# Kernel optimization log

Measured on AMD Instinct MI355X. Metric: run time of the kernel, lower is better.

## Reference

```python
import jax, jax.numpy as jnp
import numpy as np

EPS = 1e-5
HEADS = 4
DIMK = 16
DIMU = 4
R = 23


def _bn_eval(x, g, b):
    # BatchNorm2d in eval mode with running_mean=0, running_var=1
    return x * (g / np.sqrt(1.0 + EPS))[None, :, None, None] + b[None, :, None, None]


def _conv1x1(x, w):
    # w: (O, C) from a Conv2d(C, O, 1) weight
    return jnp.einsum('bchw,oc->bohw', x, w)


def _lambda_layer(x, wq, wk, wv, qg, qb, vg, vb, pw, pb):
    B, C, H, W = x.shape
    n = H * W
    V = wv.shape[0] // DIMU  # dim_out // heads
    q = _bn_eval(_conv1x1(x, wq), qg, qb).reshape(B, HEADS, DIMK, n)
    k = jax.nn.softmax(_conv1x1(x, wk).reshape(B, DIMU, DIMK, n), axis=-1)
    v = _bn_eval(_conv1x1(x, wv), vg, vb).reshape(B, DIMU, V, n)
    # content lambda: (B, k, v)
    lam_c = jnp.einsum('bukn,buvn->bkv', k, v)
    y_c = jnp.einsum('bhkn,bkv->bhvn', q, lam_c)
    # position lambdas: Conv3d(u, k, (1, R, R)) == 2D conv over (H, W) with v folded into batch
    v5 = v.reshape(B, DIMU, V, H, W).transpose(0, 2, 1, 3, 4).reshape(B * V, DIMU, H, W)
    p = R // 2
    lp = jax.lax.conv_general_dilated(v5, pw, (1, 1), [(p, p), (p, p)],
                                      dimension_numbers=('NCHW', 'OIHW', 'NCHW'))
    lp = lp + pb[None, :, None, None]
    lam_p = lp.reshape(B, V, DIMK, H, W).transpose(0, 2, 1, 3, 4).reshape(B, DIMK, V, n)
    y_p = jnp.einsum('bhkn,bkvn->bhvn', q, lam_p)
    return (y_c + y_p).reshape(B, HEADS * V, H, W)


def _group_norm(x, g, b, groups=8):
    B, C, H, W = x.shape
    xr = x.reshape(B, groups, C // groups, H, W)
    m = xr.mean(axis=(2, 3, 4), keepdims=True)
    var = xr.var(axis=(2, 3, 4), keepdims=True)
    xn = ((xr - m) / jnp.sqrt(var + EPS)).reshape(B, C, H, W)
    return xn * g[None, :, None, None] + b[None, :, None, None]


def setup_inputs() -> dict:
    key = jax.random.key(0)
    B, C, H, W = 4, 64, 192, 192
    V = C // HEADS
    d = {'x': jax.random.normal(jax.random.fold_in(key, 0), (B, C, H, W), jnp.float32)}
    i = 1
    for l in (1, 2, 3):
        for nm, shape, kind in [
            ('wq', (HEADS * DIMK, C), 'w'), ('wk', (DIMU * DIMK, C), 'w'), ('wv', (DIMU * V, C), 'w'),
            ('qg', (HEADS * DIMK,), 'ones'), ('qb', (HEADS * DIMK,), 'zeros'),
            ('vg', (DIMU * V,), 'ones'), ('vb', (DIMU * V,), 'zeros'),
            ('pw', (DIMK, DIMU, R, R), 'w'), ('pb', (DIMK,), 'zeros')]:
            if kind == 'w':
                d['l%d_%s' % (l, nm)] = jax.random.normal(jax.random.fold_in(key, i), shape, jnp.float32) * 0.05
            elif kind == 'ones':
                d['l%d_%s' % (l, nm)] = jnp.ones(shape, jnp.float32)
            else:
                d['l%d_%s' % (l, nm)] = jnp.zeros(shape, jnp.float32)
            i += 1
    d['gn1_g'] = jnp.ones((C,), jnp.float32); d['gn1_b'] = jnp.zeros((C,), jnp.float32)
    d['gn3_g'] = jnp.ones((C,), jnp.float32); d['gn3_b'] = jnp.zeros((C,), jnp.float32)
    d['cw'] = jax.random.normal(jax.random.fold_in(key, 99), (C, C), jnp.float32) * 0.01
    d['cb'] = jnp.zeros((C,), jnp.float32)
    return d


def reference(x,
              l1_wq, l1_wk, l1_wv, l1_qg, l1_qb, l1_vg, l1_vb, l1_pw, l1_pb,
              l2_wq, l2_wk, l2_wv, l2_qg, l2_qb, l2_vg, l2_vb, l2_pw, l2_pb,
              l3_wq, l3_wk, l3_wv, l3_qg, l3_qb, l3_vg, l3_vb, l3_pw, l3_pb,
              gn1_g, gn1_b, gn3_g, gn3_b, cw, cb):
    out = _lambda_layer(x, l1_wq, l1_wk, l1_wv, l1_qg, l1_qb, l1_vg, l1_vb, l1_pw, l1_pb)
    out = _group_norm(out, gn1_g, gn1_b)
    out = _lambda_layer(out, l2_wq, l2_wk, l2_wv, l2_qg, l2_qb, l2_vg, l2_vb, l2_pw, l2_pb)
    out = _group_norm(out, gn1_g, gn1_b)  # original code reuses gn1 here (gn2 unused)
    out = _lambda_layer(out, l3_wq, l3_wk, l3_wv, l3_qg, l3_qb, l3_vg, l3_vb, l3_pw, l3_pb)
    out = _group_norm(out, gn3_g, gn3_b)
    out = _conv1x1(out, cw) + cb[None, :, None, None]
    return out * 0.2 + x
```

## Files before the change

### kernel.cpp

```cpp
#include <hip/hip_runtime.h>

typedef unsigned short USH;
typedef __attribute__((ext_vector_type(8))) short bf16x8;
typedef __attribute__((ext_vector_type(4))) float f32x4;

#define MFMA16(a,b,c) __builtin_amdgcn_mfma_f32_16x16x32_bf16((a),(b),(c),0,0,0)

#define BB 4
#define HH 192
#define NN 36864
#define NTOT 147456
#define CSTR 120

__device__ __forceinline__ float bf2f(USH h) {
    union { unsigned int u; float f; } v; v.u = ((unsigned int)h) << 16; return v.f;
}
__device__ __forceinline__ USH f2bf(float f) {
    union { float f; unsigned int u; } v; v.f = f;
    unsigned int u = v.u;
    return (USH)((u + 0x7FFFu + ((u >> 16) & 1u)) >> 16);
}

struct PrepArgs {
    const float* wq[3]; const float* wk[3]; const float* wv[3];
    const float* qg[3]; const float* qb[3]; const float* vg[3]; const float* vb[3];
    const float* pw[3]; const float* cw;
};
__global__ void prep_all_k(PrepArgs pa, USH* __restrict__ apc, USH* __restrict__ apq,
                           float* __restrict__ biasq, USH* __restrict__ apf) {
    int bid = blockIdx.x, tid = threadIdx.x;
    if (bid < 552) {
        int L = bid / 184, cb = bid - L * 184;
        int t = cb * 256 + tid;
        if (t < 736 * 64) {
            const float* pw = pa.pw[L];
            USH* ap = apc + (size_t)L * 376832;
            int lane = t & 63, cg = t >> 6;
            int dy = cg % 23; int ru = cg / 23; int u = ru & 3; int r = ru >> 2;
            int kk = lane & 15, q8 = (lane >> 4) * 8;
            for (int j = 0; j < 8; ++j) {
                int k = q8 + j, dx = k - r - 1;
                USH w = 0;
                if (dx >= 0 && dx < 23) w = f2bf(pw[((kk * 4 + u) * 23 + dy) * 23 + dx]);
                ap[t * 8 + j] = w;
            }
        }
    } else if (bid < 570) {
        int idx = bid - 552; int L = idx / 6; int qblk = idx - L * 6;
        int t = qblk * 256 + tid;
        USH* apl = apq + (size_t)L * 12288;
        float* bl = biasq + L * 192;
        if (t < 1536) {
            int lane = t & 63, chunk = t >> 6;
            int mt = chunk >> 1, kc = chunk & 1;
            int o = mt * 16 + (lane & 15);
            int c0 = kc * 32 + (lane >> 4) * 8;
            float scale; const float* wrow;
            if (o < 64)       { scale = pa.qg[L][o]       * rsqrtf(1.0f + 1e-5f); wrow = pa.wq[L] + o * 64; }
            else if (o < 128) { scale = 1.0f;                                     wrow = pa.wk[L] + (o - 64) * 64; }
            else              { scale = pa.vg[L][o - 128] * rsqrtf(1.0f + 1e-5f); wrow = pa.wv[L] + (o - 128) * 64; }
            for (int j = 0; j < 8; ++j) apl[t * 8 + j] = f2bf(wrow[c0 + j] * scale);
        }
        if (t < 192) {
            float bvv;
            if (t < 64) bvv = pa.qb[L][t]; else if (t < 128) bvv = 0.0f; else bvv = pa.vb[L][t - 128];
            bl[t] = bvv;
        }
    } else {
        int t = (bid - 570) * 256 + tid;
        if (t < 512) {
            int lane = t & 63, chunk = t >> 6;
            int mt = chunk >> 1, kc = chunk & 1;
            int o = mt * 16 + (lane & 15);
            int c0 = kc * 32 + (lane >> 4) * 8;
            for (int j = 0; j < 8; ++j) apf[t * 8 + j] = f2bf(pa.cw[o * 64 + c0 + j]);
        }
    }
}

__global__ __launch_bounds__(256) void x_qkv_k(
    const float* __restrict__ xin, const bf16x8* __restrict__ apre, const float* __restrict__ bias,
    USH* __restrict__ qT, USH* __restrict__ kbuf, USH* __restrict__ vbuf) {
    __shared__ float tf[64][65];
    const int bid = blockIdx.x; const int b = bid / 576; const int nt = bid - b * 576; const int n0 = nt * 64;
    const int tid = threadIdx.x, lane = tid & 63, wq = tid >> 6;
    const int nl = lane & 15, quad = lane >> 4;
    bf16x8 afr[24];
    #pragma unroll
    for (int i = 0; i < 24; ++i) afr[i] = apre[i * 64 + lane];
    #pragma unroll
    for (int p = 0; p < 16; ++p) {
        int idx = p * 256 + tid; int c = idx >> 6, nn = idx & 63;
        tf[nn][c] = xin[((size_t)b * 64 + c) * NN + n0 + nn];
    }
    __syncthreads();
    bf16x8 b0, b1;
    #pragma unroll
    for (int j = 0; j < 8; ++j) {
        b0[j] = (short)f2bf(tf[wq * 16 + nl][quad * 8 + j]);
        b1[j] = (short)f2bf(tf[wq * 16 + nl][32 + quad * 8 + j]);
    }
    const int n = n0 + wq * 16 + nl;
    #pragma unroll
    for (int mt = 0; mt < 12; ++mt) {
        f32x4 acc = {0.f, 0.f, 0.f, 0.f};
        acc = MFMA16(afr[mt * 2 + 0], b0, acc);
        acc = MFMA16(afr[mt * 2 + 1], b1, acc);
        int o0 = mt * 16 + quad * 4;
        float4 bs = *(const float4*)(bias + o0);
        float v0 = acc[0] + bs.x, v1 = acc[1] + bs.y, v2 = acc[2] + bs.z, v3 = acc[3] + bs.w;
        if (mt < 4) {
            ushort4 pk; pk.x = f2bf(v0); pk.y = f2bf(v1); pk.z = f2bf(v2); pk.w = f2bf(v3);
            *(ushort4*)(qT + ((size_t)b * NN + n) * 64 + o0) = pk;
        } else if (mt < 8) {
            int ko = o0 - 64;
            kbuf[((size_t)b * 64 + ko    ) * NN + n] = f2bf(v0);
            kbuf[((size_t)b * 64 + ko + 1) * NN + n] = f2bf(v1);
            kbuf[((size_t)b * 64 + ko + 2) * NN + n] = f2bf(v2);
            kbuf[((size_t)b * 64 + ko + 3) * NN + n] = f2bf(v3);
        } else {
            int u = mt - 8, vv0 = quad * 4;
            vbuf[(((size_t)b * 16 + vv0    ) * 4 + u) * NN + n] = f2bf(v0);
            vbuf[(((size_t)b * 16 + vv0 + 1) * 4 + u) * NN + n] = f2bf(v1);
            vbuf[(((size_t)b * 16 + vv0 + 2) * 4 + u) * NN + n] = f2bf(v2);
            vbuf[(((size_t)b * 16 + vv0 + 3) * 4 + u) * NN + n] = f2bf(v3);
        }
    }
}

__global__ __launch_bounds__(1024) void softstat_k(const USH* __restrict__ kbuf,
                                                   float* __restrict__ kstat) {
    __shared__ USH row_s[NN];
    __shared__ float red[64];
    const USH* p = kbuf + (size_t)blockIdx.x * NN;
    int tid = threadIdx.x, lane = tid & 63, w = tid >> 6;
    float m = -1e30f;
    for (int i = tid * 4; i < NN; i += 4096) {
        ushort4 t4 = *(const ushort4*)(p + i);
        *(ushort4*)(row_s + i) = t4;
        m = fmaxf(m, fmaxf(fmaxf(bf2f(t4.x), bf2f(t4.y)), fmaxf(bf2f(t4.z), bf2f(t4.w))));
    }
    for (int off = 32; off; off >>= 1) m = fmaxf(m, __shfl_down(m, off));
    if (lane == 0) red[w] = m;
    __syncthreads();
    if (tid == 0) { float mm = red[0]; for (int i = 1; i < 16; ++i) mm = fmaxf(mm, red[i]); red[16] = mm; }
    __syncthreads();
    float M = red[16];
    float s = 0.f;
    for (int i = tid * 4; i < NN; i += 4096) {
        ushort4 t4 = *(const ushort4*)(row_s + i);
        s += __expf(bf2f(t4.x) - M) + __expf(bf2f(t4.y) - M)
           + __expf(bf2f(t4.z) - M) + __expf(bf2f(t4.w) - M);
    }
    for (int off = 32; off; off >>= 1) s += __shfl_down(s, off);
    if (lane == 0) red[32 + w] = s;
    __syncthreads();
    if (tid == 0) {
        float ss = 0.f;
        for (int i = 0; i < 16; ++i) ss += red[32 + i];
        kstat[blockIdx.x * 2]     = M;
        kstat[blockIdx.x * 2 + 1] = 1.0f / ss;
    }
}

__global__ __launch_bounds__(64) void lamc_stage1_k(
    const USH* __restrict__ kbuf, const USH* __restrict__ vbuf,
    const float* __restrict__ kstat, float* __restrict__ part) {
    int bid = blockIdx.x;
    int cidx = bid >> 4; int rem = bid & 15; int b = rem >> 2; int u = rem & 3;
    int lane = threadIdx.x; int nl = lane & 15, quad = lane >> 4;
    int krow = b * 64 + u * 16 + nl;
    float M = kstat[krow * 2], inv = kstat[krow * 2 + 1];
    const USH* kp = kbuf + (size_t)krow * NN + cidx * 512 + quad * 8;
    const USH* vp = vbuf + (((size_t)b * 16 + nl) * 4 + u) * NN + cidx * 512 + quad * 8;
    f32x4 acc = {0.f, 0.f, 0.f, 0.f};
    #pragma unroll 4
    for (int s = 0; s < 16; ++s) {
        bf16x8 kr = *(const bf16x8*)(kp + s * 32);
        bf16x8 va = *(const bf16x8*)(vp + s * 32);
        bf16x8 ka;
        #pragma unroll
        for (int j = 0; j < 8; ++j)
            ka[j] = (short)f2bf(__expf(bf2f((USH)kr[j]) - M) * inv);
        acc = MFMA16(ka, va, acc);
    }
    float* pout = part + ((size_t)(cidx * 4 + b) * 4 + u) * 256;
    #pragma unroll
    for (int rg = 0; rg < 4; ++rg)
        pout[nl * 16 + quad * 4 + rg] = acc[rg];
}
__global__ void lamc_stage2_k(const float* __restrict__ part, const float* __restrict__ pb,
                              float* __restrict__ lamcf) {
    int b = blockIdx.x, tid = threadIdx.x;
    float acc = 0.f;
    for (int c = 0; c < 72; ++c)
        for (int u = 0; u < 4; ++u)
            acc += part[((size_t)(c * 4 + b) * 4 + u) * 256 + tid];
    lamcf[b * 256 + tid] = acc + pb[tid & 15];
}

__global__ __launch_bounds__(256, 3) void conv_pos_fused_k(
    const USH* __restrict__ vbuf, const bf16x8* __restrict__ apre,
    const USH* __restrict__ qT, const float* __restrict__ lamcf,
    USH* __restrict__ yb, float* __restrict__ gnp2) {
    __shared__ __align__(16) USH in_s[4 * 54 * CSTR];
    __shared__ float lc_s[16];
    __shared__ float gn_s[16], gn_q[16];
    const int xh = blockIdx.x, yt = blockIdx.y, img = blockIdx.z;
    const int b = img >> 4, vvch = img & 15;
    const int tid = threadIdx.x;
    if (tid < 16) lc_s[tid] = lamcf[b * 256 + vvch * 16 + tid];
    {
        const USH* vb = vbuf + (size_t)img * 4 * NN;
        const int y0 = yt * 32 - 11, x0 = xh * 96 - 12;
        for (int i4 = tid; i4 < 6480; i4 += 256) {
            int u = i4 / 1620;
            int rem = i4 - u * 1620;
            int rr = rem / 30;
            int cc = (rem - rr * 30) * 4;
            int gy = y0 + rr, gx = x0 + cc;
            ushort4 val = {0, 0, 0, 0};
            if (gy >= 0 && gy < HH && gx >= 0 && gx <= HH - 4)
                val = *(const ushort4*)(vb + u * NN + gy * HH + gx);
            *(ushort4*)(in_s + (u * 54 + rr) * CSTR + cc) = val;
        }
    }
    __syncthreads();

    const int lane = tid & 63, wv = tid >> 6;
    const int wy = wv >> 1, wx = wv & 1;
    const int nl = lane & 15, quad = lane >> 4;
    const USH* sbase = in_s + (wy * 16 + nl) * CSTR + wx * 48 + quad * 8;
    const int ybase = yt * 32 + wy * 16 + nl;
    float lcr0 = lc_s[quad * 4], lcr1 = lc_s[quad * 4 + 1],
          lcr2 = lc_s[quad * 4 + 2], lcr3 = lc_s[quad * 4 + 3];
    const USH* qbase = qT + ((size_t)b * NN + ybase * HH) * 64 + quad * 4;
    USH* ybbase = yb + ((size_t)b * 64 + quad * 16 + vvch) * NN + ybase * HH;
    float SG = 0.f, QG = 0.f;

#define CONV_EPILOGUE(ACC, RVAL)                                                            \
    {                                                                                       \
        _Pragma("unroll")                                                                   \
        for (int xi = 0; xi < 6; ++xi) {                                                    \
            int x = xh * 96 + wx * 48 + (RVAL) + 8 * xi;                                    \
            float l0 = ACC[xi][0] + lcr0, l1 = ACC[xi][1] + lcr1;                           \
            float l2 = ACC[xi][2] + lcr2, l3 = ACC[xi][3] + lcr3;                           \
            const USH* qp = qbase + (size_t)x * 64;                                         \
            float s0, s1, s2, s3;                                                           \
            {                                                                               \
                ushort4 q4 = *(const ushort4*)(qp);                                         \
                s0 = bf2f(q4.x) * l0 + bf2f(q4.y) * l1 + bf2f(q4.z) * l2 + bf2f(q4.w) * l3; \
            }                                                                               \
            {                                                                               \
                ushort4 q4 = *(const ushort4*)(qp + 16);                                    \
                s1 = bf2f(q4.x) * l0 + bf2f(q4.y) * l1 + bf2f(q4.z) * l2 + bf2f(q4.w) * l3; \
            }                                                                               \
            {                                                                               \
                ushort4 q4 = *(const ushort4*)(qp + 32);                                    \
                s2 = bf2f(q4.x) * l0 + bf2f(q4.y) * l1 + bf2f(q4.z) * l2 + bf2f(q4.w) * l3; \
            }                                                                               \
            {                                                                               \
                ushort4 q4 = *(const ushort4*)(qp + 48);                                    \
                s3 = bf2f(q4.x) * l0 + bf2f(q4.y) * l1 + bf2f(q4.z) * l2 + bf2f(q4.w) * l3; \
            }                                                                               \
            s0 += __shfl_xor(s0, 16); s0 += __shfl_xor(s0, 32);                             \
            s1 += __shfl_xor(s1, 16); s1 += __shfl_xor(s1, 32);                             \
            s2 += __shfl_xor(s2, 16); s2 += __shfl_xor(s2, 32);                             \
            s3 += __shfl_xor(s3, 16); s3 += __shfl_xor(s3, 32);                             \
            float sel = (quad == 0) ? s0 : (quad == 1) ? s1 : (quad == 2) ? s2 : s3;        \
            USH wo = f2bf(sel);                                                             \
            ybbase[x] = wo;                                                                 \
            float wf = bf2f(wo);                                                            \
            SG += wf; QG += wf * wf;                                                        \
        }                                                                                   \
    }

#define CONV_PASS3(R0)                                                                      \
    {                                                                                       \
        f32x4 acc0[6] = {}; f32x4 acc1[6] = {}; f32x4 acc2[6] = {};                         \
        for (int u = 0; u < 4; ++u) {                                                       \
            const bf16x8* ap0 = apre + ((size_t)((R0) * 4 + u) * 23) * 64 + lane;           \
            const bf16x8* ap1 = ap0 + 4 * 23 * 64;                                          \
            const bf16x8* ap2 = ap0 + 2 * 4 * 23 * 64;                                      \
            const USH* srow = sbase + u * (54 * CSTR);                                      \
            _Pragma("unroll 2")                                                             \
            for (int dy = 0; dy < 23; ++dy) {                                               \
                bf16x8 a0 = *ap0, a1 = *ap1, a2 = *ap2;                                     \
                _Pragma("unroll")                                                           \
                for (int xi = 0; xi < 6; ++xi) {                                            \
                    bf16x8 bfr = *(const bf16x8*)(srow + 8 * xi);                           \
                    acc0[xi] = MFMA16(a0, bfr, acc0[xi]);                                   \
                    acc1[xi] = MFMA16(a1, bfr, acc1[xi]);                                   \
                    acc2[xi] = MFMA16(a2, bfr, acc2[xi]);                                   \
                }                                                                           \
                ap0 += 64; ap1 += 64; ap2 += 64; srow += CSTR;                               \
            }                                                                               \
        }                                                                                   \
        CONV_EPILOGUE(acc0, (R0))                                                           \
        CONV_EPILOGUE(acc1, (R0) + 1)                                                       \
        CONV_EPILOGUE(acc2, (R0) + 2)                                                       \
    }

    CONV_PASS3(0)
    CONV_PASS3(3)
    {
        f32x4 acc0[6] = {}; f32x4 acc1[6] = {};
        for (int u = 0; u < 4; ++u) {
            const bf16x8* ap0 = apre + ((size_t)(6 * 4 + u) * 23) * 64 + lane;
            const bf16x8* ap1 = ap0 + 4 * 23 * 64;
            const USH* srow = sbase + u * (54 * CSTR);
            #pragma unroll 2
            for (int dy = 0; dy < 23; ++dy) {
                bf16x8 a0 = *ap0, a1 = *ap1;
                #pragma unroll
                for (int xi = 0; xi < 6; ++xi) {
                    bf16x8 bfr = *(const bf16x8*)(srow + 8 * xi);
                    acc0[xi] = MFMA16(a0, bfr, acc0[xi]);
                    acc1[xi] = MFMA16(a1, bfr, acc1[xi]);
                }
                ap0 += 64; ap1 += 64; srow += CSTR;
            }
        }
        CONV_EPILOGUE(acc0, 6)
        CONV_EPILOGUE(acc1, 7)
    }
#undef CONV_PASS3
#undef CONV_EPILOGUE

    SG += __shfl_xor(SG, 1); SG += __shfl_xor(SG, 2); SG += __shfl_xor(SG, 4); SG += __shfl_xor(SG, 8);
    QG += __shfl_xor(QG, 1); QG += __shfl_xor(QG, 2); QG += __shfl_xor(QG, 4); QG += __shfl_xor(QG, 8);
    if (nl == 0) { gn_s[wv * 4 + quad] = SG; gn_q[wv * 4 + quad] = QG; }
    __syncthreads();
    if (tid < 4) {
        float s = gn_s[tid] + gn_s[4 + tid] + gn_s[8 + tid] + gn_s[12 + tid];
        float q = gn_q[tid] + gn_q[4 + tid] + gn_q[8 + tid] + gn_q[12 + tid];
        int lin = img * 12 + yt * 2 + xh;
        gnp2[lin * 8 + tid * 2]     = s;
        gnp2[lin * 8 + tid * 2 + 1] = q;
    }
}

__global__ void gn_passB_k(const float* __restrict__ gnp2, float* __restrict__ stats) {
    int t = threadIdx.x;
    if (t < 32) {
        int b = t >> 3, g = t & 7;
        int quad = g >> 1, v0 = (g & 1) * 8;
        float s = 0.f, q = 0.f;
        for (int vv = 0; vv < 8; ++vv)
            for (int tile = 0; tile < 12; ++tile) {
                const float* p = gnp2 + ((size_t)((b * 16 + v0 + vv) * 12 + tile)) * 8 + quad * 2;
                s += p[0]; q += p[1];
            }
        float mean = s / 294912.0f;
        float var = q / 294912.0f - mean * mean;
        stats[t * 2] = mean;
        stats[t * 2 + 1] = rsqrtf(fmaxf(var, 0.0f) + 1e-5f);
    }
}

__global__ __launch_bounds__(256) void gn_qkv_k(
    const USH* __restrict__ yb, const float* __restrict__ stats,
    const float* __restrict__ gg, const float* __restrict__ gb,
    const bf16x8* __restrict__ apre, const float* __restrict__ bias,
    USH* __restrict__ qT, USH* __restrict__ kbuf, USH* __restrict__ vbuf) {
    __shared__ float tf[64][65];
    __shared__ float sc[64], sb[64];
    const int bid = blockIdx.x; const int b = bid / 576; const int nt = bid - b * 576; const int n0 = nt * 64;
    const int tid = threadIdx.x, lane = tid & 63, wq = tid >> 6;
    const int nl = lane & 15, quad = lane >> 4;
    bf16x8 afr[24];
    #pragma unroll
    for (int i = 0; i < 24; ++i) afr[i] = apre[i * 64 + lane];
    if (tid < 64) {
        int g = tid >> 3;
        float mean = stats[(b * 8 + g) * 2], rstd = stats[(b * 8 + g) * 2 + 1];
        float ga = gg[tid];
        sc[tid] = rstd * ga;
        sb[tid] = gb[tid] - mean * rstd * ga;
    }
    __syncthreads();
    #pragma unroll
    for (int p = 0; p < 4; ++p) {
        int c = p * 16 + (tid >> 4), nn = (tid & 15) * 4;
        ushort4 y4 = *(const ushort4*)(yb + ((size_t)b * 64 + c) * NN + n0 + nn);
        float scc = sc[c], sbc = sb[c];
        tf[nn][c]     = bf2f(y4.x) * scc + sbc;
        tf[nn + 1][c] = bf2f(y4.y) * scc + sbc;
        tf[nn + 2][c] = bf2f(y4.z) * scc + sbc;
        tf[nn + 3][c] = bf2f(y4.w) * scc + sbc;
    }
    __syncthreads();
    bf16x8 b0, b1;
    #pragma unroll
    for (int j = 0; j < 8; ++j) {
        b0[j] = (short)f2bf(tf[wq * 16 + nl][quad * 8 + j]);
        b1[j] = (short)f2bf(tf[wq * 16 + nl][32 + quad * 8 + j]);
    }
    const int n = n0 + wq * 16 + nl;
    #pragma unroll
    for (int mt = 0; mt < 12; ++mt) {
        f32x4 acc = {0.f, 0.f, 0.f, 0.f};
        acc = MFMA16(afr[mt * 2 + 0], b0, acc);
        acc = MFMA16(afr[mt * 2 + 1], b1, acc);
        int o0 = mt * 16 + quad * 4;
        float4 bs = *(const float4*)(bias + o0);
        float v0 = acc[0] + bs.x, v1 = acc[1] + bs.y, v2 = acc[2] + bs.z, v3 = acc[3] + bs.w;
        if (mt < 4) {
            ushort4 pk; pk.x = f2bf(v0); pk.y = f2bf(v1); pk.z = f2bf(v2); pk.w = f2bf(v3);
            *(ushort4*)(qT + ((size_t)b * NN + n) * 64 + o0) = pk;
        } else if (mt < 8) {
            int ko = o0 - 64;
            kbuf[((size_t)b * 64 + ko    ) * NN + n] = f2bf(v0);
            kbuf[((size_t)b * 64 + ko + 1) * NN + n] = f2bf(v1);
            kbuf[((size_t)b * 64 + ko + 2) * NN + n] = f2bf(v2);
            kbuf[((size_t)b * 64 + ko + 3) * NN + n] = f2bf(v3);
        } else {
            int u = mt - 8, vv0 = quad * 4;
            vbuf[(((size_t)b * 16 + vv0    ) * 4 + u) * NN + n] = f2bf(v0);
            vbuf[(((size_t)b * 16 + vv0 + 1) * 4 + u) * NN + n] = f2bf(v1);
            vbuf[(((size_t)b * 16 + vv0 + 2) * 4 + u) * NN + n] = f2bf(v2);
            vbuf[(((size_t)b * 16 + vv0 + 3) * 4 + u) * NN + n] = f2bf(v3);
        }
    }
}

__global__ __launch_bounds__(256) void gn_final_k(
    const USH* __restrict__ yb, const float* __restrict__ stats,
    const float* __restrict__ gg, const float* __restrict__ gb,
    const bf16x8* __restrict__ apre, const float* __restrict__ cb,
    const float* __restrict__ xin, float* __restrict__ out) {
    __shared__ float tf[64][65];
    __shared__ float sc[64], sb[64];
    const int bid = blockIdx.x; const int b = bid / 576; const int nt = bid - b * 576; const int n0 = nt * 64;
    const int tid = threadIdx.x, lane = tid & 63, wq = tid >> 6;
    const int nl = lane & 15, quad = lane >> 4;
    bf16x8 afr[8];
    #pragma unroll
    for (int i = 0; i < 8; ++i) afr[i] = apre[i * 64 + lane];
    if (tid < 64) {
        int g = tid >> 3;
        float mean = stats[(b * 8 + g) * 2], rstd = stats[(b * 8 + g) * 2 + 1];
        float ga = gg[tid];
        sc[tid] = rstd * ga;
        sb[tid] = gb[tid] - mean * rstd * ga;
    }
    __syncthreads();
    #pragma unroll
    for (int p = 0; p < 4; ++p) {
        int c = p * 16 + (tid >> 4), nn = (tid & 15) * 4;
        ushort4 y4 = *(const ushort4*)(yb + ((size_t)b * 64 + c) * NN + n0 + nn);
        float scc = sc[c], sbc = sb[c];
        tf[nn][c]     = bf2f(y4.x) * scc + sbc;
        tf[nn + 1][c] = bf2f(y4.y) * scc + sbc;
        tf[nn + 2][c] = bf2f(y4.z) * scc + sbc;
        tf[nn + 3][c] = bf2f(y4.w) * scc + sbc;
    }
    __syncthreads();
    bf16x8 b0, b1;
    #pragma unroll
    for (int j = 0; j < 8; ++j) {
        b0[j] = (short)f2bf(tf[wq * 16 + nl][quad * 8 + j]);
        b1[j] = (short)f2bf(tf[wq * 16 + nl][32 + quad * 8 + j]);
    }
    const int n = n0 + wq * 16 + nl;
    #pragma unroll
    for (int mt = 0; mt < 4; ++mt) {
        f32x4 acc = {0.f, 0.f, 0.f, 0.f};
        acc = MFMA16(afr[mt * 2 + 0], b0, acc);
        acc = MFMA16(afr[mt * 2 + 1], b1, acc);
        int o0 = mt * 16 + quad * 4;
        float4 cb4 = *(const float4*)(cb + o0);
        float cbv[4] = { cb4.x, cb4.y, cb4.z, cb4.w };
        #pragma unroll
        for (int rg = 0; rg < 4; ++rg) {
            int o = o0 + rg;
            float xv = xin[((size_t)b * 64 + o) * NN + n];
            out[((size_t)b * 64 + o) * NN + n] = (acc[rg] + cbv[rg]) * 0.2f + xv;
        }
    }
}

extern "C" void kernel_launch(void* const* d_in, const int* in_sizes, int n_in,
                              void* d_out, int out_size, void* d_ws, size_t ws_size,
                              hipStream_t stream) {
    (void)in_sizes; (void)n_in; (void)out_size; (void)ws_size;
    const float* x = (const float*)d_in[0];
    char* ws = (char*)d_ws;

    const size_t SZP = (size_t)NTOT * 64 * 2;
    USH*   P0 = (USH*)(ws);
    USH*   P1 = (USH*)(ws + SZP);
    USH*   P2 = (USH*)(ws + 2 * SZP);
    USH*   P3 = (USH*)(ws + 3 * SZP);
    char*  tail  = ws + 4 * SZP;
    USH*   apc   = (USH*)(tail);            tail += 753664 * 3;
    USH*   apq   = (USH*)(tail);            tail += 24576 * 3;
    float* biasq = (float*)(tail);          tail += 768 * 3;
    USH*   apf   = (USH*)(tail);            tail += 8192;
    float* lcp   = (float*)(tail);          tail += 1179648;
    float* lcf   = (float*)(tail);          tail += 4096;
    float* gnp2  = (float*)(tail);          tail += 24576;
    float* gns   = (float*)(tail);          tail += 256;
    float* kst   = (float*)(tail);

    PrepArgs pa;
    for (int L = 0; L < 3; ++L) {
        int base = 1 + L * 9;
        pa.wq[L] = (const float*)d_in[base + 0];
        pa.wk[L] = (const float*)d_in[base + 1];
        pa.wv[L] = (const float*)d_in[base + 2];
        pa.qg[L] = (const float*)d_in[base + 3];
        pa.qb[L] = (const float*)d_in[base + 4];
        pa.vg[L] = (const float*)d_in[base + 5];
        pa.vb[L] = (const float*)d_in[base + 6];
        pa.pw[L] = (const float*)d_in[base + 7];
    }
    pa.cw = (const float*)d_in[32];

    prep_all_k<<<572, 256, 0, stream>>>(pa, apc, apq, biasq, apf);

    x_qkv_k<<<2304, 256, 0, stream>>>(x, (const bf16x8*)apq, biasq, P1, P2, P3);

    for (int L = 0; L < 3; ++L) {
        const float* pb = (const float*)d_in[1 + L * 9 + 8];
        USH* kv = (L == 1) ? P0 : P2;

        softstat_k<<<256, 1024, 0, stream>>>(kv, kst);
        lamc_stage1_k<<<1152, 64, 0, stream>>>(kv, P3, kst, lcp);
        lamc_stage2_k<<<4, 256, 0, stream>>>(lcp, pb, lcf);
        dim3 cg(2, 6, 64);
        conv_pos_fused_k<<<cg, 256, 0, stream>>>(P3, (const bf16x8*)apc + (size_t)L * 47104,
                                                 P1, lcf, kv, gnp2);
        gn_passB_k<<<1, 256, 0, stream>>>(gnp2, gns);
        if (L < 2) {
            const float* gg = (const float*)d_in[28];
            const float* gb = (const float*)d_in[29];
            USH* knext = (L == 0) ? P0 : P2;
            gn_qkv_k<<<2304, 256, 0, stream>>>(kv, gns, gg, gb,
                                               (const bf16x8*)apq + (size_t)(L + 1) * 1536,
                                               biasq + (L + 1) * 192, P1, knext, P3);
        } else {
            const float* gg = (const float*)d_in[30];
            const float* gb = (const float*)d_in[31];
            gn_final_k<<<2304, 256, 0, stream>>>(kv, gns, gg, gb, (const bf16x8*)apf,
                                                 (const float*)d_in[33], x, (float*)d_out);
        }
    }
}
```

Measured before the change: 942.1 us.

## Fold lambda-content and group-norm reductions into consumer kernels, drop tiny launches

Removes the single-block lamc_stage2 and gn_passB kernels per layer. Their reductions now run redundantly inside every conv_pos_fused and gn_qkv/gn_final block. lamc_stage1 is split into 192 chunks instead of 72 to raise parallelism, which enlarges the partial buffer. The aim is to remove serialized tiny launches and their pipeline bubbles, at the cost of redundant global reads of the partials in every consumer block.

```diff
diff --git a/kernel.cpp b/kernel.cpp
--- a/kernel.cpp
+++ b/kernel.cpp
@@ -11,6 +11,7 @@
 #define NN 36864
 #define NTOT 147456
 #define CSTR 120
+#define NCH 192
 
 __device__ __forceinline__ float bf2f(USH h) {
     union { unsigned int u; float f; } v; v.u = ((unsigned int)h) << 16; return v.f;
@@ -171,11 +172,11 @@
     int lane = threadIdx.x; int nl = lane & 15, quad = lane >> 4;
     int krow = b * 64 + u * 16 + nl;
     float M = kstat[krow * 2], inv = kstat[krow * 2 + 1];
-    const USH* kp = kbuf + (size_t)krow * NN + cidx * 512 + quad * 8;
-    const USH* vp = vbuf + (((size_t)b * 16 + nl) * 4 + u) * NN + cidx * 512 + quad * 8;
+    const USH* kp = kbuf + (size_t)krow * NN + cidx * 192 + quad * 8;
+    const USH* vp = vbuf + (((size_t)b * 16 + nl) * 4 + u) * NN + cidx * 192 + quad * 8;
     f32x4 acc = {0.f, 0.f, 0.f, 0.f};
-    #pragma unroll 4
-    for (int s = 0; s < 16; ++s) {
+    #pragma unroll
+    for (int s = 0; s < 6; ++s) {
         bf16x8 kr = *(const bf16x8*)(kp + s * 32);
         bf16x8 va = *(const bf16x8*)(vp + s * 32);
         bf16x8 ka;
@@ -189,27 +190,27 @@
     for (int rg = 0; rg < 4; ++rg)
         pout[nl * 16 + quad * 4 + rg] = acc[rg];
 }
-__global__ void lamc_stage2_k(const float* __restrict__ part, const float* __restrict__ pb,
-                              float* __restrict__ lamcf) {
-    int b = blockIdx.x, tid = threadIdx.x;
-    float acc = 0.f;
-    for (int c = 0; c < 72; ++c)
-        for (int u = 0; u < 4; ++u)
-            acc += part[((size_t)(c * 4 + b) * 4 + u) * 256 + tid];
-    lamcf[b * 256 + tid] = acc + pb[tid & 15];
-}
 
 __global__ __launch_bounds__(256, 3) void conv_pos_fused_k(
     const USH* __restrict__ vbuf, const bf16x8* __restrict__ apre,
-    const USH* __restrict__ qT, const float* __restrict__ lamcf,
-    USH* __restrict__ yb, float* __restrict__ gnp2) {
+    const USH* __restrict__ qT, const float* __restrict__ lcp,
+    const float* __restrict__ pb, USH* __restrict__ yb, float* __restrict__ gnp2) {
     __shared__ __align__(16) USH in_s[4 * 54 * CSTR];
+    __shared__ float lc_red[16][16];
     __shared__ float lc_s[16];
     __shared__ float gn_s[16], gn_q[16];
     const int xh = blockIdx.x, yt = blockIdx.y, img = blockIdx.z;
     const int b = img >> 4, vvch = img & 15;
     const int tid = threadIdx.x;
-    if (tid < 16) lc_s[tid] = lamcf[b * 256 + vvch * 16 + tid];
+    {
+        int kk = tid & 15, slice = tid >> 4;
+        float s = 0.f;
+        for (int p = slice * 48; p < slice * 48 + 48; ++p) {
+            int cidx = p >> 2, u = p & 3;
+            s += lcp[((size_t)(cidx * 4 + b) * 4 + u) * 256 + vvch * 16 + kk];
+        }
+        lc_red[slice][kk] = s;
+    }
     {
         const USH* vb = vbuf + (size_t)img * 4 * NN;
         const int y0 = yt * 32 - 11, x0 = xh * 96 - 12;
@@ -224,6 +225,13 @@
                 val = *(const ushort4*)(vb + u * NN + gy * HH + gx);
             *(ushort4*)(in_s + (u * 54 + rr) * CSTR + cc) = val;
         }
+    }
+    __syncthreads();
+    if (tid < 16) {
+        float s = 0.f;
+        #pragma unroll
+        for (int sl = 0; sl < 16; ++sl) s += lc_red[sl][tid];
+        lc_s[tid] = s + pb[tid];
     }
     __syncthreads();
 
@@ -340,31 +348,14 @@
     }
 }
 
-__global__ void gn_passB_k(const float* __restrict__ gnp2, float* __restrict__ stats) {
-    int t = threadIdx.x;
-    if (t < 32) {
-        int b = t >> 3, g = t & 7;
-        int quad = g >> 1, v0 = (g & 1) * 8;
-        float s = 0.f, q = 0.f;
-        for (int vv = 0; vv < 8; ++vv)
-            for (int tile = 0; tile < 12; ++tile) {
-                const float* p = gnp2 + ((size_t)((b * 16 + v0 + vv) * 12 + tile)) * 8 + quad * 2;
-                s += p[0]; q += p[1];
-            }
-        float mean = s / 294912.0f;
-        float var = q / 294912.0f - mean * mean;
-        stats[t * 2] = mean;
-        stats[t * 2 + 1] = rsqrtf(fmaxf(var, 0.0f) + 1e-5f);
-    }
-}
-
 __global__ __launch_bounds__(256) void gn_qkv_k(
-    const USH* __restrict__ yb, const float* __restrict__ stats,
+    const USH* __restrict__ yb, const float* __restrict__ gnp2,
     const float* __restrict__ gg, const float* __restrict__ gb,
     const bf16x8* __restrict__ apre, const float* __restrict__ bias,
     USH* __restrict__ qT, USH* __restrict__ kbuf, USH* __restrict__ vbuf) {
     __shared__ float tf[64][65];
     __shared__ float sc[64], sb[64];
+    __shared__ float grs[64], grq[64], st_s[16];
     const int bid = blockIdx.x; const int b = bid / 576; const int nt = bid - b * 576; const int n0 = nt * 64;
     const int tid = threadIdx.x, lane = tid & 63, wq = tid >> 6;
     const int nl = lane & 15, quad = lane >> 4;
@@ -372,8 +363,30 @@
     #pragma unroll
     for (int i = 0; i < 24; ++i) afr[i] = apre[i * 64 + lane];
     if (tid < 64) {
+        int g = tid >> 3, vv = tid & 7;
+        int qg = g >> 1, v0 = (g & 1) * 8;
+        float s = 0.f, q = 0.f;
+        #pragma unroll
+        for (int tile = 0; tile < 12; ++tile) {
+            const float* p = gnp2 + ((size_t)((b * 16 + v0 + vv) * 12 + tile)) * 8 + qg * 2;
+            s += p[0]; q += p[1];
+        }
+        grs[tid] = s; grq[tid] = q;
+    }
+    __syncthreads();
+    if (tid < 8) {
+        float s = 0.f, q = 0.f;
+        #pragma unroll
+        for (int vv = 0; vv < 8; ++vv) { s += grs[tid * 8 + vv]; q += grq[tid * 8 + vv]; }
+        float mean = s / 294912.0f;
+        float var = q / 294912.0f - mean * mean;
+        st_s[tid * 2] = mean;
+        st_s[tid * 2 + 1] = rsqrtf(fmaxf(var, 0.0f) + 1e-5f);
+    }
+    __syncthreads();
+    if (tid < 64) {
         int g = tid >> 3;
-        float mean = stats[(b * 8 + g) * 2], rstd = stats[(b * 8 + g) * 2 + 1];
+        float mean = st_s[g * 2], rstd = st_s[g * 2 + 1];
         float ga = gg[tid];
         sc[tid] = rstd * ga;
         sb[tid] = gb[tid] - mean * rstd * ga;
@@ -425,12 +438,13 @@
 }
 
 __global__ __launch_bounds__(256) void gn_final_k(
-    const USH* __restrict__ yb, const float* __restrict__ stats,
+    const USH* __restrict__ yb, const float* __restrict__ gnp2,
     const float* __restrict__ gg, const float* __restrict__ gb,
     const bf16x8* __restrict__ apre, const float* __restrict__ cb,
     const float* __restrict__ xin, float* __restrict__ out) {
     __shared__ float tf[64][65];
     __shared__ float sc[64], sb[64];
+    __shared__ float grs[64], grq[64], st_s[16];
     const int bid = blockIdx.x; const int b = bid / 576; const int nt = bid - b * 576; const int n0 = nt * 64;
     const int tid = threadIdx.x, lane = tid & 63, wq = tid >> 6;
     const int nl = lane & 15, quad = lane >> 4;
@@ -438,8 +452,30 @@
     #pragma unroll
     for (int i = 0; i < 8; ++i) afr[i] = apre[i * 64 + lane];
     if (tid < 64) {
+        int g = tid >> 3, vv = tid & 7;
+        int qg = g >> 1, v0 = (g & 1) * 8;
+        float s = 0.f, q = 0.f;
+        #pragma unroll
+        for (int tile = 0; tile < 12; ++tile) {
+            const float* p = gnp2 + ((size_t)((b * 16 + v0 + vv) * 12 + tile)) * 8 + qg * 2;
+            s += p[0]; q += p[1];
+        }
+        grs[tid] = s; grq[tid] = q;
+    }
+    __syncthreads();
+    if (tid < 8) {
+        float s = 0.f, q = 0.f;
+        #pragma unroll
+        for (int vv = 0; vv < 8; ++vv) { s += grs[tid * 8 + vv]; q += grq[tid * 8 + vv]; }
+        float mean = s / 294912.0f;
+        float var = q / 294912.0f - mean * mean;
+        st_s[tid * 2] = mean;
+        st_s[tid * 2 + 1] = rsqrtf(fmaxf(var, 0.0f) + 1e-5f);
+    }
+    __syncthreads();
+    if (tid < 64) {
         int g = tid >> 3;
-        float mean = stats[(b * 8 + g) * 2], rstd = stats[(b * 8 + g) * 2 + 1];
+        float mean = st_s[g * 2], rstd = st_s[g * 2 + 1];
         float ga = gg[tid];
         sc[tid] = rstd * ga;
         sb[tid] = gb[tid] - mean * rstd * ga;
@@ -497,10 +533,8 @@
     USH*   apq   = (USH*)(tail);            tail += 24576 * 3;
     float* biasq = (float*)(tail);          tail += 768 * 3;
     USH*   apf   = (USH*)(tail);            tail += 8192;
-    float* lcp   = (float*)(tail);          tail += 1179648;
-    float* lcf   = (float*)(tail);          tail += 4096;
+    float* lcp   = (float*)(tail);          tail += 3145728;
     float* gnp2  = (float*)(tail);          tail += 24576;
-    float* gns   = (float*)(tail);          tail += 256;
     float* kst   = (float*)(tail);
 
     PrepArgs pa;
@@ -526,23 +560,21 @@
         USH* kv = (L == 1) ? P0 : P2;
 
         softstat_k<<<256, 1024, 0, stream>>>(kv, kst);
-        lamc_stage1_k<<<1152, 64, 0, stream>>>(kv, P3, kst, lcp);
-        lamc_stage2_k<<<4, 256, 0, stream>>>(lcp, pb, lcf);
+        lamc_stage1_k<<<NCH * 16, 64, 0, stream>>>(kv, P3, kst, lcp);
         dim3 cg(2, 6, 64);
         conv_pos_fused_k<<<cg, 256, 0, stream>>>(P3, (const bf16x8*)apc + (size_t)L * 47104,
-                                                 P1, lcf, kv, gnp2);
-        gn_passB_k<<<1, 256, 0, stream>>>(gnp2, gns);
+                                                 P1, lcp, pb, kv, gnp2);
         if (L < 2) {
             const float* gg = (const float*)d_in[28];
             const float* gb = (const float*)d_in[29];
             USH* knext = (L == 0) ? P0 : P2;
-            gn_qkv_k<<<2304, 256, 0, stream>>>(kv, gns, gg, gb,
+            gn_qkv_k<<<2304, 256, 0, stream>>>(kv, gnp2, gg, gb,
                                                (const bf16x8*)apq + (size_t)(L + 1) * 1536,
                                                biasq + (L + 1) * 192, P1, knext, P3);
         } else {
             const float* gg = (const float*)d_in[30];
             const float* gb = (const float*)d_in[31];
-            gn_final_k<<<2304, 256, 0, stream>>>(kv, gns, gg, gb, (const bf16x8*)apf,
+            gn_final_k<<<2304, 256, 0, stream>>>(kv, gnp2, gg, gb, (const bf16x8*)apf,
                                                  (const float*)d_in[33], x, (float*)d_out);
         }
     }
```

New measurement: 909.3 us. 3.5% less time.
